# Kernel optimization log

Measured on AMD Instinct MI355X. Metric: run time of the kernel, lower is better.

Reference implementation:

```python
import jax, jax.numpy as jnp
import numpy as np

HEADS = 6
WIN = 7
SHIFT = 3
NEG = -100.0


def _rel_index():
    # Swin relative position index, [49, 49] int
    coords = np.stack(np.meshgrid(np.arange(WIN), np.arange(WIN), indexing='ij')).reshape(2, -1)
    rel = (coords[:, :, None] - coords[:, None, :]).transpose(1, 2, 0)
    rel[:, :, 0] += WIN - 1
    rel[:, :, 1] += WIN - 1
    rel[:, :, 0] *= 2 * WIN - 1
    return rel.sum(-1)


def _shift_mask(H, W):
    # additive shift mask per window, [num_windows, 49, 49]
    img = np.zeros([H, W])
    slices = (slice(0, -WIN), slice(-WIN, -SHIFT), slice(-SHIFT, None))
    cnt = 0
    for h in slices:
        for w in slices:
            img[h, w] = cnt
            cnt += 1
    mw = img.reshape(H // WIN, WIN, W // WIN, WIN).transpose(0, 2, 1, 3).reshape(-1, WIN * WIN)
    diff = mw[:, None, :] - mw[:, :, None]
    return np.where(diff != 0, NEG, 0.0).astype(np.float32)


def setup_inputs() -> dict:
    key = jax.random.key(0)
    ks = jax.random.split(key, 6)
    B, H, W, C = 64, 56, 56, 192
    return {
        'x': jax.random.normal(ks[0], (B, H, W, C), jnp.float32),
        'qkv_w': jax.random.normal(ks[1], (C, 3 * C), jnp.float32) * 0.02,
        'qkv_b': jax.random.normal(ks[2], (3 * C,), jnp.float32) * 0.02,
        'rel_table': jax.random.normal(ks[3], ((2 * WIN - 1) ** 2, HEADS), jnp.float32) * 0.02,
        'proj_w': jax.random.normal(ks[4], (C, C), jnp.float32) * 0.02,
        'proj_b': jax.random.normal(ks[5], (C,), jnp.float32) * 0.02,
    }


def reference(x, qkv_w, qkv_b, rel_table, proj_w, proj_b):
    B, H, W, C = x.shape
    hd = C // HEADS
    scale = hd ** -0.5
    mask = jnp.asarray(_shift_mask(H, W))            # [nW, N, N]
    idx = _rel_index().reshape(-1)                   # static numpy [N*N]

    # cyclic shift + window partition
    xs = jnp.roll(x, (-SHIFT, -SHIFT), (1, 2))
    xw = xs.reshape(B, H // WIN, WIN, W // WIN, WIN, C)
    xw = xw.transpose(0, 1, 3, 2, 4, 5).reshape(-1, WIN * WIN, C)  # [Bn, N, C]
    Bn, N, _ = xw.shape

    qkv = (xw @ qkv_w + qkv_b).reshape(Bn, N, 3, HEADS, hd).transpose(2, 0, 3, 1, 4)
    q, k, v = qkv[0] * scale, qkv[1], qkv[2]         # [Bn, h, N, hd]

    attn = jax.nn.softmax(jnp.einsum('bhnd,bhmd->bhnm', q, k), axis=-1)

    # NOTE: original module adds relative bias and shift mask AFTER softmax
    bias = rel_table[idx].reshape(N, N, HEADS).transpose(2, 0, 1)  # [h, N, N]
    attn = attn + bias[None]
    nW = mask.shape[0]
    attn = (attn.reshape(Bn // nW, nW, HEADS, N, N) + mask[None, :, None]).reshape(Bn, HEADS, N, N)

    out = jnp.einsum('bhnm,bhmd->bhnd', attn, v).transpose(0, 2, 1, 3).reshape(Bn, N, C)
    out = out @ proj_w + proj_b

    # window reverse + un-shift
    out = out.reshape(B, H // WIN, W // WIN, WIN, WIN, C)
    out = out.transpose(0, 1, 3, 2, 4, 5).reshape(B, H, W, C)
    return jnp.roll(out, (SHIFT, SHIFT), (1, 2))
```

## Files before the change

kernel.cpp:

```cpp
#include <hip/hip_runtime.h>
#include <hip/hip_bf16.h>

typedef __attribute__((ext_vector_type(8))) short bf16x8_t;
typedef __attribute__((ext_vector_type(4))) short bf16x4_t;
typedef __attribute__((ext_vector_type(4))) float f32x4_t;

#define MFMA16 __builtin_amdgcn_mfma_f32_16x16x32_bf16

#if __has_builtin(__builtin_amdgcn_mfma_f32_16x16x16bf16_1k)
#define HAVE_MFMA_K16 1
#define MFMA16K16 __builtin_amdgcn_mfma_f32_16x16x16bf16_1k
#else
#define HAVE_MFMA_K16 0
#endif

__device__ __forceinline__ unsigned short f2bf(float f) {
    return __builtin_bit_cast(unsigned short, __float2bfloat16(f));
}
__device__ __forceinline__ int cvt_pk_bf16(float lo, float hi) {
    int r;
    asm("v_cvt_pk_bf16_f32 %0, %1, %2" : "=v"(r) : "v"(lo), "v"(hi));
    return r;
}

__device__ __forceinline__ void group_barrier(int* cnt, int target, int ln) {
    asm volatile("s_waitcnt lgkmcnt(0)" ::: "memory");
    if (ln == 0)
        __hip_atomic_fetch_add(cnt, 1, __ATOMIC_RELEASE, __HIP_MEMORY_SCOPE_WORKGROUP);
    while (__hip_atomic_load(cnt, __ATOMIC_ACQUIRE, __HIP_MEMORY_SCOPE_WORKGROUP) < target)
        __builtin_amdgcn_s_sleep(1);
    __builtin_amdgcn_sched_barrier(0);
}

#define GRP_STRIDE 49152
#define ROWOFF_OFF 98304
#define BAR_OFF    98816
#define SMEM_BYTES 98832

__device__ __forceinline__ int qk_byte(int row, int d) {
    return row * 64 + ((((d >> 3) ^ ((row >> 1) & 3)) << 4) | ((d & 7) << 1));
}
__device__ __forceinline__ int vt_byte(int d, int tok) {
    return d * 128 + ((((tok >> 3) ^ (d & 7)) << 4) | ((tok & 7) << 1));
}

__global__ void prep_weights(const float* __restrict__ qkv_w, const float* __restrict__ proj_w,
                             unsigned short* __restrict__ wqkvT, unsigned short* __restrict__ wprojT)
{
    int i = blockIdx.x * 256 + threadIdx.x;
    if (i < 576 * 192) {
        int n = i / 192, k = i - n * 192;
        wqkvT[i] = f2bf(qkv_w[k * 576 + n]);
    }
    if (i < 192 * 192) {
        int n = i / 192, k = i - n * 192;
        wprojT[i] = f2bf(proj_w[k * 192 + n]);
    }
}

__global__ void prep_bias(const float* __restrict__ rel_table, float* __restrict__ biasT)
{
    int i = blockIdx.x * 256 + threadIdx.x;
    if (i >= 4 * 6 * 16 * 64) return;
    int ln  = i & 63;
    int f   = (i >> 6) & 15;
    int h   = (i >> 10) % 6;
    int wt  = i / 6144;
    int l15 = ln & 15, lg = ln >> 4;
    int mk  = f >> 2, nq = f & 3;
    int qt  = nq * 16 + l15;
    bool bh = (wt & 2) != 0, bw = (wt & 1) != 0;
    float4 o = {0.f, 0.f, 0.f, 0.f};
    float* po = (float*)&o;
    int iq = qt / 7, jq = qt - iq * 7;
    int regq = (bh ? ((iq < 4) ? 3 : 6) : 0) + (bw ? ((jq < 4) ? 1 : 2) : 0);
    for (int r = 0; r < 4; ++r) {
        int kt = mk * 16 + lg * 4 + r;
        if (kt < 49 && qt < 49) {
            int ik = kt / 7, jk = kt - ik * 7;
            int idx = (iq - ik + 6) * 13 + (jq - jk + 6);
            int regk = (bh ? ((ik < 4) ? 3 : 6) : 0) + (bw ? ((jk < 4) ? 1 : 2) : 0);
            po[r] = rel_table[idx * 6 + h] + ((regk != regq) ? -100.0f : 0.0f);
        }
    }
    ((float4*)biasT)[i] = o;
}

__global__ __launch_bounds__(768, 3)
void swin_fused(const float* __restrict__ x,
                const float* __restrict__ qkv_b,
                const float* __restrict__ proj_b,
                const unsigned short* __restrict__ wqkvT,
                const unsigned short* __restrict__ wprojT,
                const float* __restrict__ biasT,
                float* __restrict__ out)
{
    __shared__ unsigned char smem[SMEM_BYTES];

    const int tid = threadIdx.x;
    const int wv  = tid >> 6;
    const int g   = (wv >= 6) ? 1 : 0;
    const int h   = wv - 6 * g;
    const int ln  = tid & 63;
    const int l15 = ln & 15;
    const int lg  = ln >> 4;
    const int tg  = tid - g * 384;

    const int bw  = blockIdx.x * 2 + g;
    const int b   = bw >> 6;
    const int win = bw & 63;
    const int wh  = win >> 3;
    const int ww  = win & 7;
    const int wt  = ((wh == 7) ? 2 : 0) | ((ww == 7) ? 1 : 0);

    const unsigned gbase = g * GRP_STRIDE;
    const unsigned hbase = gbase + h * 8192;
    int* rowOff = (int*)(smem + ROWOFF_OFF + g * 256);
    int* bar    = (int*)(smem + BAR_OFF) + g;
    const f32x4_t zero4 = {0.f, 0.f, 0.f, 0.f};

    if (tid < 2) ((int*)(smem + BAR_OFF))[tid] = 0;
    __syncthreads();

#pragma unroll
    for (int it = 0; it < 8; ++it) {
        int idx = tg + it * 384;
        int n   = idx / 48;
        int c4  = idx - n * 48;
        int2* dst = (int2*)(smem + gbase + n * 400 + c4 * 8);
        if (n < 49) {
            int i = n / 7, j = n - i * 7;
            int sh = wh * 7 + i + 3; if (sh >= 56) sh -= 56;
            int sw = ww * 7 + j + 3; if (sw >= 56) sw -= 56;
            int ro = ((b * 56 + sh) * 56 + sw) * 192;
            if (c4 == 0) rowOff[n] = ro;
            const float4* src = (const float4*)(x + ro + c4 * 4);
            float4 v = *src;
            int2 p;
            p.x = cvt_pk_bf16(v.x, v.y);
            p.y = cvt_pk_bf16(v.z, v.w);
            *dst = p;
        } else {
            *dst = make_int2(0, 0);
        }
    }
    group_barrier(bar, 6, ln);

    f32x4_t accq[4][6];
#pragma unroll
    for (int mt = 0; mt < 4; ++mt)
#pragma unroll
        for (int nt = 0; nt < 6; ++nt) accq[mt][nt] = zero4;
#pragma unroll
    for (int ks = 0; ks < 6; ++ks) {
        bf16x8_t af[4];
#pragma unroll
        for (int mt = 0; mt < 4; ++mt)
            af[mt] = *(const bf16x8_t*)(smem + gbase + (mt * 16 + l15) * 400 + (ks * 32 + lg * 8) * 2);
        bf16x8_t bfv[6];
#pragma unroll
        for (int nt = 0; nt < 6; ++nt)
            bfv[nt] = *(const bf16x8_t*)(wqkvT + ((nt >> 1) * 192 + h * 32 + (nt & 1) * 16 + l15) * 192 + ks * 32 + lg * 8);
        __builtin_amdgcn_s_setprio(1);
#pragma unroll
        for (int nt = 0; nt < 6; ++nt)
#pragma unroll
            for (int mt = 0; mt < 4; ++mt)
                accq[mt][nt] = MFMA16(af[mt], bfv[nt], accq[mt][nt], 0, 0, 0);
        __builtin_amdgcn_s_setprio(0);
    }
    int vbf[4][2][2];
#pragma unroll
    for (int nv = 0; nv < 2; ++nv) {
        float bb = qkv_b[384 + h * 32 + nv * 16 + l15];
#pragma unroll
        for (int mt = 0; mt < 4; ++mt) {
            vbf[mt][nv][0] = cvt_pk_bf16(accq[mt][4 + nv][0] + bb, accq[mt][4 + nv][1] + bb);
            vbf[mt][nv][1] = cvt_pk_bf16(accq[mt][4 + nv][2] + bb, accq[mt][4 + nv][3] + bb);
        }
    }
    group_barrier(bar, 12, ln);

#pragma unroll
    for (int nt = 0; nt < 4; ++nt) {
        int part = nt >> 1;
        int d    = (nt & 1) * 16 + l15;
        float bb = qkv_b[part * 192 + h * 32 + d];
        unsigned base = hbase + part * 4096;
#pragma unroll
        for (int mt = 0; mt < 4; ++mt)
#pragma unroll
            for (int r = 0; r < 4; ++r) {
                int row = mt * 16 + lg * 4 + r;
                *(unsigned short*)(smem + base + qk_byte(row, d)) = f2bf(accq[mt][nt][r] + bb);
            }
    }
    __builtin_amdgcn_sched_barrier(0);

    f32x4_t s[4][4];
    {
        bf16x8_t kf[4], qf[4];
#pragma unroll
        for (int mk = 0; mk < 4; ++mk) {
            int row = mk * 16 + l15;
            kf[mk] = *(const bf16x8_t*)(smem + hbase + 4096 + row * 64 + ((lg ^ ((row >> 1) & 3)) << 4));
        }
#pragma unroll
        for (int nq = 0; nq < 4; ++nq) {
            int row = nq * 16 + l15;
            qf[nq] = *(const bf16x8_t*)(smem + hbase + row * 64 + ((lg ^ ((row >> 1) & 3)) << 4));
        }
        __builtin_amdgcn_s_setprio(1);
#pragma unroll
        for (int mk = 0; mk < 4; ++mk)
#pragma unroll
            for (int nq = 0; nq < 4; ++nq)
                s[mk][nq] = MFMA16(kf[mk], qf[nq], zero4, 0, 0, 0);
        __builtin_amdgcn_s_setprio(0);
    }
    __builtin_amdgcn_sched_barrier(0);

#pragma unroll
    for (int nv = 0; nv < 2; ++nv) {
        int d = nv * 16 + l15;
#pragma unroll
        for (int mt = 0; mt < 4; ++mt) {
            int tok = mt * 16 + lg * 4;
            *(int2*)(smem + hbase + vt_byte(d, tok)) = make_int2(vbf[mt][nv][0], vbf[mt][nv][1]);
        }
    }

    float4 bv4[4][4];
    {
        const float4* bp = (const float4*)biasT + (wt * 6 + h) * 16 * 64 + ln;
#pragma unroll
        for (int mk = 0; mk < 4; ++mk)
#pragma unroll
            for (int nq = 0; nq < 4; ++nq)
                bv4[mk][nq] = bp[(mk * 4 + nq) * 64];
    }

    const float C = 0.17677669529663687f * 1.4426950408889634f;
    int w[4][4][2];
#pragma unroll
    for (int nq = 0; nq < 4; ++nq) {
        float sum = 0.f;
#pragma unroll
        for (int mk = 0; mk < 4; ++mk)
#pragma unroll
            for (int r = 0; r < 4; ++r) {
                int kt = mk * 16 + lg * 4 + r;
                float e = (kt < 49) ? __builtin_amdgcn_exp2f(C * s[mk][nq][r]) : 0.0f;
                s[mk][nq][r] = e;
                sum += e;
            }
        sum += __shfl_xor(sum, 16);
        sum += __shfl_xor(sum, 32);
        float inv = __builtin_amdgcn_rcpf(sum);
#pragma unroll
        for (int mk = 0; mk < 4; ++mk) {
            float v0 = fmaf(s[mk][nq][0], inv, bv4[mk][nq].x);
            float v1 = fmaf(s[mk][nq][1], inv, bv4[mk][nq].y);
            float v2 = fmaf(s[mk][nq][2], inv, bv4[mk][nq].z);
            float v3 = fmaf(s[mk][nq][3], inv, bv4[mk][nq].w);
            w[mk][nq][0] = cvt_pk_bf16(v0, v1);
            w[mk][nq][1] = cvt_pk_bf16(v2, v3);
        }
    }

    f32x4_t o[2][4];
#pragma unroll
    for (int md = 0; md < 2; ++md)
#pragma unroll
        for (int nq = 0; nq < 4; ++nq) o[md][nq] = zero4;

#if HAVE_MFMA_K16
#pragma unroll
    for (int mk = 0; mk < 4; ++mk) {
        bf16x4_t vt2[2];
#pragma unroll
        for (int md = 0; md < 2; ++md) {
            int d = md * 16 + l15;
            vt2[md] = *(const bf16x4_t*)(smem + hbase + vt_byte(d, mk * 16 + lg * 4));
        }
        __builtin_amdgcn_s_setprio(1);
#pragma unroll
        for (int nq = 0; nq < 4; ++nq) {
            bf16x4_t wb = __builtin_bit_cast(bf16x4_t, make_int2(w[mk][nq][0], w[mk][nq][1]));
#pragma unroll
            for (int md = 0; md < 2; ++md)
                o[md][nq] = MFMA16K16(vt2[md], wb, o[md][nq], 0, 0, 0);
        }
        __builtin_amdgcn_s_setprio(0);
    }
#else
    const unsigned Abase = hbase + 4096;
#pragma unroll
    for (int ks = 0; ks < 2; ++ks) {
#pragma unroll
        for (int mh = 0; mh < 2; ++mh) {
            int mk = ks * 2 + mh;
            int d  = mh * 16 + lg * 4;
#pragma unroll
            for (int nq = 0; nq < 4; ++nq) {
                int qt = nq * 16 + l15;
                *(int2*)(smem + Abase + qk_byte(qt, d)) = make_int2(w[mk][nq][0], w[mk][nq][1]);
            }
        }
        __builtin_amdgcn_sched_barrier(0);
        bf16x8_t vf[2], bfr[4];
#pragma unroll
        for (int md = 0; md < 2; ++md) {
            int d = md * 16 + l15;
            vf[md] = *(const bf16x8_t*)(smem + hbase + d * 128 + (((ks * 4 + lg) ^ (d & 7)) << 4));
        }
#pragma unroll
        for (int nq = 0; nq < 4; ++nq) {
            int qt = nq * 16 + l15;
            bfr[nq] = *(const bf16x8_t*)(smem + Abase + qt * 64 + ((lg ^ ((qt >> 1) & 3)) << 4));
        }
        __builtin_amdgcn_s_setprio(1);
#pragma unroll
        for (int nq = 0; nq < 4; ++nq)
#pragma unroll
            for (int md = 0; md < 2; ++md)
                o[md][nq] = MFMA16(vf[md], bfr[nq], o[md][nq], 0, 0, 0);
        __builtin_amdgcn_s_setprio(0);
        __builtin_amdgcn_sched_barrier(0);
    }
#endif
    group_barrier(bar, 18, ln);

#pragma unroll
    for (int md = 0; md < 2; ++md)
#pragma unroll
        for (int nq = 0; nq < 4; ++nq) {
            int qt = nq * 16 + l15;
            int ch = h * 32 + md * 16 + lg * 4;
            int d0 = cvt_pk_bf16(o[md][nq][0], o[md][nq][1]);
            int d1 = cvt_pk_bf16(o[md][nq][2], o[md][nq][3]);
            *(int2*)(smem + gbase + qt * 400 + ch * 2) = make_int2(d0, d1);
        }
    group_barrier(bar, 24, ln);

    f32x4_t y[4][2];
#pragma unroll
    for (int mt = 0; mt < 4; ++mt) { y[mt][0] = zero4; y[mt][1] = zero4; }
#pragma unroll
    for (int ks = 0; ks < 6; ++ks) {
        bf16x8_t aa[4], bb[2];
#pragma unroll
        for (int mt = 0; mt < 4; ++mt)
            aa[mt] = *(const bf16x8_t*)(smem + gbase + (mt * 16 + l15) * 400 + (ks * 32 + lg * 8) * 2);
#pragma unroll
        for (int nt = 0; nt < 2; ++nt)
            bb[nt] = *(const bf16x8_t*)(wprojT + (h * 32 + nt * 16 + l15) * 192 + ks * 32 + lg * 8);
        __builtin_amdgcn_s_setprio(1);
#pragma unroll
        for (int mt = 0; mt < 4; ++mt)
#pragma unroll
            for (int nt = 0; nt < 2; ++nt)
                y[mt][nt] = MFMA16(aa[mt], bb[nt], y[mt][nt], 0, 0, 0);
        __builtin_amdgcn_s_setprio(0);
    }
    float pb0 = proj_b[h * 32 + l15];
    float pb1 = proj_b[h * 32 + 16 + l15];
#pragma unroll
    for (int mt = 0; mt < 4; ++mt)
#pragma unroll
        for (int r = 0; r < 4; ++r) {
            int row = mt * 16 + lg * 4 + r;
            if (row < 49) {
                int ro = rowOff[row];
                out[ro + h * 32 + l15]      = y[mt][0][r] + pb0;
                out[ro + h * 32 + 16 + l15] = y[mt][1][r] + pb1;
            }
        }
}

extern "C" void kernel_launch(void* const* d_in, const int* in_sizes, int n_in,
                              void* d_out, int out_size, void* d_ws, size_t ws_size,
                              hipStream_t stream) {
    const float* x         = (const float*)d_in[0];
    const float* qkv_w     = (const float*)d_in[1];
    const float* qkv_b     = (const float*)d_in[2];
    const float* rel_table = (const float*)d_in[3];
    const float* proj_w    = (const float*)d_in[4];
    const float* proj_b    = (const float*)d_in[5];
    float* out = (float*)d_out;

    unsigned short* wqkvT  = (unsigned short*)d_ws;
    unsigned short* wprojT = wqkvT + 576 * 192;
    float* biasT = (float*)((char*)d_ws + 294912);

    prep_weights<<<576, 256, 0, stream>>>(qkv_w, proj_w, wqkvT, wprojT);
    prep_bias<<<96, 256, 0, stream>>>(rel_table, biasT);
    swin_fused<<<2048, 768, 0, stream>>>(x, qkv_b, proj_b, wqkvT, wprojT, biasT, out);
}
```

Before: 231.5 us.

## Make fused Swin kernel persistent with register prefetch of next window input

The launch shrinks from 2048 to 256 blocks, and each block loops over 8 batch images for the same pair of windows. A separate LDS buffer for the x tile plus a double-buffered row-offset table lets the global loads for the next iteration be issued into registers during the current iteration's output and projection phase. The intent is to hide global load latency and spread launch and setup cost over more work. In exchange, LDS use grows to about 150KB (one block per CU), register pressure rises from the 8 float4 prefetch registers, and only 256 blocks run, which may under-fill the GPU.

```diff
diff --git a/kernel.cpp b/kernel.cpp
--- a/kernel.cpp
+++ b/kernel.cpp
@@ -32,10 +32,11 @@
     __builtin_amdgcn_sched_barrier(0);
 }
 
-#define GRP_STRIDE 49152
-#define ROWOFF_OFF 98304
-#define BAR_OFF    98816
-#define SMEM_BYTES 98832
+#define XB_OFF     98304
+#define ROWOFF_OFF 149504
+#define BAR_OFF    150528
+#define SMEM_BYTES 150536
+#define NIT 8
 
 __device__ __forceinline__ int qk_byte(int row, int d) {
     return row * 64 + ((((d >> 3) ^ ((row >> 1) & 3)) << 4) | ((d & 7) << 1));
@@ -106,276 +107,301 @@
     const int lg  = ln >> 4;
     const int tg  = tid - g * 384;
 
-    const int bw  = blockIdx.x * 2 + g;
-    const int b   = bw >> 6;
-    const int win = bw & 63;
+    const int bx2 = blockIdx.x * 2 + g;
+    const int b0  = bx2 >> 6;
+    const int win = bx2 & 63;
     const int wh  = win >> 3;
     const int ww  = win & 7;
     const int wt  = ((wh == 7) ? 2 : 0) | ((ww == 7) ? 1 : 0);
 
-    const unsigned gbase = g * GRP_STRIDE;
+    const unsigned gbase = g * 49152;
     const unsigned hbase = gbase + h * 8192;
-    int* rowOff = (int*)(smem + ROWOFF_OFF + g * 256);
-    int* bar    = (int*)(smem + BAR_OFF) + g;
+    const unsigned xb    = XB_OFF + g * 25600;
+    int* bar = (int*)(smem + BAR_OFF) + g;
     const f32x4_t zero4 = {0.f, 0.f, 0.f, 0.f};
+    const float4* bp = (const float4*)biasT + (wt * 6 + h) * 16 * 64 + ln;
 
     if (tid < 2) ((int*)(smem + BAR_OFF))[tid] = 0;
     __syncthreads();
 
 #pragma unroll
-    for (int it = 0; it < 8; ++it) {
-        int idx = tg + it * 384;
+    for (int c = 0; c < 8; ++c) {
+        int idx = tg + c * 384;
         int n   = idx / 48;
         int c4  = idx - n * 48;
-        int2* dst = (int2*)(smem + gbase + n * 400 + c4 * 8);
-        if (n < 49) {
-            int i = n / 7, j = n - i * 7;
-            int sh = wh * 7 + i + 3; if (sh >= 56) sh -= 56;
-            int sw = ww * 7 + j + 3; if (sw >= 56) sw -= 56;
-            int ro = ((b * 56 + sh) * 56 + sw) * 192;
-            if (c4 == 0) rowOff[n] = ro;
-            const float4* src = (const float4*)(x + ro + c4 * 4);
-            float4 v = *src;
-            int2 p;
-            p.x = cvt_pk_bf16(v.x, v.y);
-            p.y = cvt_pk_bf16(v.z, v.w);
-            *dst = p;
-        } else {
-            *dst = make_int2(0, 0);
-        }
+        if (n >= 49) *(int2*)(smem + xb + n * 400 + c4 * 8) = make_int2(0, 0);
     }
-    group_barrier(bar, 6, ln);
-
-    f32x4_t accq[4][6];
-#pragma unroll
-    for (int mt = 0; mt < 4; ++mt)
-#pragma unroll
-        for (int nt = 0; nt < 6; ++nt) accq[mt][nt] = zero4;
-#pragma unroll
-    for (int ks = 0; ks < 6; ++ks) {
-        bf16x8_t af[4];
+
+    float4 xr[8];
+    auto prefetch = [&](int itn) {
+        const int bn = itn * 8 + b0;
+        int* rowOffN = (int*)(smem + ROWOFF_OFF + (g * 2 + (itn & 1)) * 256);
+#pragma unroll
+        for (int c = 0; c < 8; ++c) {
+            int idx = tg + c * 384;
+            int n   = idx / 48;
+            int c4  = idx - n * 48;
+            if (n < 49) {
+                int i = n / 7, j = n - i * 7;
+                int sh = wh * 7 + i + 3; if (sh >= 56) sh -= 56;
+                int sw = ww * 7 + j + 3; if (sw >= 56) sw -= 56;
+                int ro = ((bn * 56 + sh) * 56 + sw) * 192;
+                if (c4 == 0) rowOffN[n] = ro;
+                xr[c] = *(const float4*)(x + ro + c4 * 4);
+            }
+        }
+    };
+    prefetch(0);
+
+#pragma unroll 1
+    for (int it = 0; it < NIT; ++it) {
+        const int p  = it & 1;
+        const int tb = it * 18;
+
+#pragma unroll
+        for (int c = 0; c < 8; ++c) {
+            int idx = tg + c * 384;
+            int n   = idx / 48;
+            int c4  = idx - n * 48;
+            if (n < 49) {
+                int2 pk;
+                pk.x = cvt_pk_bf16(xr[c].x, xr[c].y);
+                pk.y = cvt_pk_bf16(xr[c].z, xr[c].w);
+                *(int2*)(smem + xb + n * 400 + c4 * 8) = pk;
+            }
+        }
+        group_barrier(bar, tb + 6, ln);
+
+        f32x4_t accq[4][6];
 #pragma unroll
         for (int mt = 0; mt < 4; ++mt)
-            af[mt] = *(const bf16x8_t*)(smem + gbase + (mt * 16 + l15) * 400 + (ks * 32 + lg * 8) * 2);
-        bf16x8_t bfv[6];
-#pragma unroll
-        for (int nt = 0; nt < 6; ++nt)
-            bfv[nt] = *(const bf16x8_t*)(wqkvT + ((nt >> 1) * 192 + h * 32 + (nt & 1) * 16 + l15) * 192 + ks * 32 + lg * 8);
-        __builtin_amdgcn_s_setprio(1);
-#pragma unroll
-        for (int nt = 0; nt < 6; ++nt)
+#pragma unroll
+            for (int nt = 0; nt < 6; ++nt) accq[mt][nt] = zero4;
+#pragma unroll
+        for (int ks = 0; ks < 6; ++ks) {
+            bf16x8_t af[4];
 #pragma unroll
             for (int mt = 0; mt < 4; ++mt)
-                accq[mt][nt] = MFMA16(af[mt], bfv[nt], accq[mt][nt], 0, 0, 0);
-        __builtin_amdgcn_s_setprio(0);
-    }
-    int vbf[4][2][2];
-#pragma unroll
-    for (int nv = 0; nv < 2; ++nv) {
-        float bb = qkv_b[384 + h * 32 + nv * 16 + l15];
-#pragma unroll
-        for (int mt = 0; mt < 4; ++mt) {
-            vbf[mt][nv][0] = cvt_pk_bf16(accq[mt][4 + nv][0] + bb, accq[mt][4 + nv][1] + bb);
-            vbf[mt][nv][1] = cvt_pk_bf16(accq[mt][4 + nv][2] + bb, accq[mt][4 + nv][3] + bb);
-        }
-    }
-    group_barrier(bar, 12, ln);
-
-#pragma unroll
-    for (int nt = 0; nt < 4; ++nt) {
-        int part = nt >> 1;
-        int d    = (nt & 1) * 16 + l15;
-        float bb = qkv_b[part * 192 + h * 32 + d];
-        unsigned base = hbase + part * 4096;
+                af[mt] = *(const bf16x8_t*)(smem + xb + (mt * 16 + l15) * 400 + (ks * 32 + lg * 8) * 2);
+            bf16x8_t bfv[6];
+#pragma unroll
+            for (int nt = 0; nt < 6; ++nt)
+                bfv[nt] = *(const bf16x8_t*)(wqkvT + ((nt >> 1) * 192 + h * 32 + (nt & 1) * 16 + l15) * 192 + ks * 32 + lg * 8);
+            __builtin_amdgcn_s_setprio(1);
+#pragma unroll
+            for (int nt = 0; nt < 6; ++nt)
+#pragma unroll
+                for (int mt = 0; mt < 4; ++mt)
+                    accq[mt][nt] = MFMA16(af[mt], bfv[nt], accq[mt][nt], 0, 0, 0);
+            __builtin_amdgcn_s_setprio(0);
+        }
+        int vbf[4][2][2];
+#pragma unroll
+        for (int nv = 0; nv < 2; ++nv) {
+            float bb = qkv_b[384 + h * 32 + nv * 16 + l15];
+#pragma unroll
+            for (int mt = 0; mt < 4; ++mt) {
+                vbf[mt][nv][0] = cvt_pk_bf16(accq[mt][4 + nv][0] + bb, accq[mt][4 + nv][1] + bb);
+                vbf[mt][nv][1] = cvt_pk_bf16(accq[mt][4 + nv][2] + bb, accq[mt][4 + nv][3] + bb);
+            }
+        }
+
+#pragma unroll
+        for (int nt = 0; nt < 4; ++nt) {
+            int part = nt >> 1;
+            int d    = (nt & 1) * 16 + l15;
+            float bb = qkv_b[part * 192 + h * 32 + d];
+            unsigned base = hbase + part * 4096;
+#pragma unroll
+            for (int mt = 0; mt < 4; ++mt)
+#pragma unroll
+                for (int r = 0; r < 4; ++r) {
+                    int row = mt * 16 + lg * 4 + r;
+                    *(unsigned short*)(smem + base + qk_byte(row, d)) = f2bf(accq[mt][nt][r] + bb);
+                }
+        }
+        __builtin_amdgcn_sched_barrier(0);
+
+        f32x4_t s[4][4];
+        {
+            bf16x8_t kf[4], qf[4];
+#pragma unroll
+            for (int mk = 0; mk < 4; ++mk) {
+                int row = mk * 16 + l15;
+                kf[mk] = *(const bf16x8_t*)(smem + hbase + 4096 + row * 64 + ((lg ^ ((row >> 1) & 3)) << 4));
+            }
+#pragma unroll
+            for (int nq = 0; nq < 4; ++nq) {
+                int row = nq * 16 + l15;
+                qf[nq] = *(const bf16x8_t*)(smem + hbase + row * 64 + ((lg ^ ((row >> 1) & 3)) << 4));
+            }
+            __builtin_amdgcn_s_setprio(1);
+#pragma unroll
+            for (int mk = 0; mk < 4; ++mk)
+#pragma unroll
+                for (int nq = 0; nq < 4; ++nq)
+                    s[mk][nq] = MFMA16(kf[mk], qf[nq], zero4, 0, 0, 0);
+            __builtin_amdgcn_s_setprio(0);
+        }
+        __builtin_amdgcn_sched_barrier(0);
+
+#pragma unroll
+        for (int nv = 0; nv < 2; ++nv) {
+            int d = nv * 16 + l15;
+#pragma unroll
+            for (int mt = 0; mt < 4; ++mt) {
+                int tok = mt * 16 + lg * 4;
+                *(int2*)(smem + hbase + vt_byte(d, tok)) = make_int2(vbf[mt][nv][0], vbf[mt][nv][1]);
+            }
+        }
+
+        float4 bv4[4][4];
+#pragma unroll
+        for (int mk = 0; mk < 4; ++mk)
+#pragma unroll
+            for (int nq = 0; nq < 4; ++nq)
+                bv4[mk][nq] = bp[(mk * 4 + nq) * 64];
+
+        const float C = 0.17677669529663687f * 1.4426950408889634f;
+        int w[4][4][2];
+#pragma unroll
+        for (int nq = 0; nq < 4; ++nq) {
+            float sum = 0.f;
+#pragma unroll
+            for (int mk = 0; mk < 4; ++mk)
+#pragma unroll
+                for (int r = 0; r < 4; ++r) {
+                    int kt = mk * 16 + lg * 4 + r;
+                    float e = (kt < 49) ? __builtin_amdgcn_exp2f(C * s[mk][nq][r]) : 0.0f;
+                    s[mk][nq][r] = e;
+                    sum += e;
+                }
+            sum += __shfl_xor(sum, 16);
+            sum += __shfl_xor(sum, 32);
+            float inv = __builtin_amdgcn_rcpf(sum);
+#pragma unroll
+            for (int mk = 0; mk < 4; ++mk) {
+                float v0 = fmaf(s[mk][nq][0], inv, bv4[mk][nq].x);
+                float v1 = fmaf(s[mk][nq][1], inv, bv4[mk][nq].y);
+                float v2 = fmaf(s[mk][nq][2], inv, bv4[mk][nq].z);
+                float v3 = fmaf(s[mk][nq][3], inv, bv4[mk][nq].w);
+                w[mk][nq][0] = cvt_pk_bf16(v0, v1);
+                w[mk][nq][1] = cvt_pk_bf16(v2, v3);
+            }
+        }
+
+        f32x4_t o[2][4];
+#pragma unroll
+        for (int md = 0; md < 2; ++md)
+#pragma unroll
+            for (int nq = 0; nq < 4; ++nq) o[md][nq] = zero4;
+
+#if HAVE_MFMA_K16
+#pragma unroll
+        for (int mk = 0; mk < 4; ++mk) {
+            bf16x4_t vt2[2];
+#pragma unroll
+            for (int md = 0; md < 2; ++md) {
+                int d = md * 16 + l15;
+                vt2[md] = *(const bf16x4_t*)(smem + hbase + vt_byte(d, mk * 16 + lg * 4));
+            }
+            __builtin_amdgcn_s_setprio(1);
+#pragma unroll
+            for (int nq = 0; nq < 4; ++nq) {
+                bf16x4_t wb = __builtin_bit_cast(bf16x4_t, make_int2(w[mk][nq][0], w[mk][nq][1]));
+#pragma unroll
+                for (int md = 0; md < 2; ++md)
+                    o[md][nq] = MFMA16K16(vt2[md], wb, o[md][nq], 0, 0, 0);
+            }
+            __builtin_amdgcn_s_setprio(0);
+        }
+#else
+        const unsigned Abase = hbase + 4096;
+#pragma unroll
+        for (int ks = 0; ks < 2; ++ks) {
+#pragma unroll
+            for (int mh = 0; mh < 2; ++mh) {
+                int mk = ks * 2 + mh;
+                int d  = mh * 16 + lg * 4;
+#pragma unroll
+                for (int nq = 0; nq < 4; ++nq) {
+                    int qt = nq * 16 + l15;
+                    *(int2*)(smem + Abase + qk_byte(qt, d)) = make_int2(w[mk][nq][0], w[mk][nq][1]);
+                }
+            }
+            __builtin_amdgcn_sched_barrier(0);
+            bf16x8_t vf[2], bfr[4];
+#pragma unroll
+            for (int md = 0; md < 2; ++md) {
+                int d = md * 16 + l15;
+                vf[md] = *(const bf16x8_t*)(smem + hbase + d * 128 + (((ks * 4 + lg) ^ (d & 7)) << 4));
+            }
+#pragma unroll
+            for (int nq = 0; nq < 4; ++nq) {
+                int qt = nq * 16 + l15;
+                bfr[nq] = *(const bf16x8_t*)(smem + Abase + qt * 64 + ((lg ^ ((qt >> 1) & 3)) << 4));
+            }
+            __builtin_amdgcn_s_setprio(1);
+#pragma unroll
+            for (int nq = 0; nq < 4; ++nq)
+#pragma unroll
+                for (int md = 0; md < 2; ++md)
+                    o[md][nq] = MFMA16(vf[md], bfr[nq], o[md][nq], 0, 0, 0);
+            __builtin_amdgcn_s_setprio(0);
+            __builtin_amdgcn_sched_barrier(0);
+        }
+#endif
+        group_barrier(bar, tb + 12, ln);
+
+        if (it + 1 < NIT) prefetch(it + 1);
+
+#pragma unroll
+        for (int md = 0; md < 2; ++md)
+#pragma unroll
+            for (int nq = 0; nq < 4; ++nq) {
+                int qt = nq * 16 + l15;
+                int ch = h * 32 + md * 16 + lg * 4;
+                int d0 = cvt_pk_bf16(o[md][nq][0], o[md][nq][1]);
+                int d1 = cvt_pk_bf16(o[md][nq][2], o[md][nq][3]);
+                *(int2*)(smem + gbase + qt * 400 + ch * 2) = make_int2(d0, d1);
+            }
+        group_barrier(bar, tb + 18, ln);
+
+        f32x4_t y[4][2];
+#pragma unroll
+        for (int mt = 0; mt < 4; ++mt) { y[mt][0] = zero4; y[mt][1] = zero4; }
+#pragma unroll
+        for (int ks = 0; ks < 6; ++ks) {
+            bf16x8_t aa[4], bb[2];
+#pragma unroll
+            for (int mt = 0; mt < 4; ++mt)
+                aa[mt] = *(const bf16x8_t*)(smem + gbase + (mt * 16 + l15) * 400 + (ks * 32 + lg * 8) * 2);
+#pragma unroll
+            for (int nt = 0; nt < 2; ++nt)
+                bb[nt] = *(const bf16x8_t*)(wprojT + (h * 32 + nt * 16 + l15) * 192 + ks * 32 + lg * 8);
+            __builtin_amdgcn_s_setprio(1);
+#pragma unroll
+            for (int mt = 0; mt < 4; ++mt)
+#pragma unroll
+                for (int nt = 0; nt < 2; ++nt)
+                    y[mt][nt] = MFMA16(aa[mt], bb[nt], y[mt][nt], 0, 0, 0);
+            __builtin_amdgcn_s_setprio(0);
+        }
+        int* rowOff = (int*)(smem + ROWOFF_OFF + (g * 2 + p) * 256);
+        float pb0 = proj_b[h * 32 + l15];
+        float pb1 = proj_b[h * 32 + 16 + l15];
 #pragma unroll
         for (int mt = 0; mt < 4; ++mt)
 #pragma unroll
             for (int r = 0; r < 4; ++r) {
                 int row = mt * 16 + lg * 4 + r;
-                *(unsigned short*)(smem + base + qk_byte(row, d)) = f2bf(accq[mt][nt][r] + bb);
+                if (row < 49) {
+                    int ro = rowOff[row];
+                    out[ro + h * 32 + l15]      = y[mt][0][r] + pb0;
+                    out[ro + h * 32 + 16 + l15] = y[mt][1][r] + pb1;
+                }
             }
     }
-    __builtin_amdgcn_sched_barrier(0);
-
-    f32x4_t s[4][4];
-    {
-        bf16x8_t kf[4], qf[4];
-#pragma unroll
-        for (int mk = 0; mk < 4; ++mk) {
-            int row = mk * 16 + l15;
-            kf[mk] = *(const bf16x8_t*)(smem + hbase + 4096 + row * 64 + ((lg ^ ((row >> 1) & 3)) << 4));
-        }
-#pragma unroll
-        for (int nq = 0; nq < 4; ++nq) {
-            int row = nq * 16 + l15;
-            qf[nq] = *(const bf16x8_t*)(smem + hbase + row * 64 + ((lg ^ ((row >> 1) & 3)) << 4));
-        }
-        __builtin_amdgcn_s_setprio(1);
-#pragma unroll
-        for (int mk = 0; mk < 4; ++mk)
-#pragma unroll
-            for (int nq = 0; nq < 4; ++nq)
-                s[mk][nq] = MFMA16(kf[mk], qf[nq], zero4, 0, 0, 0);
-        __builtin_amdgcn_s_setprio(0);
-    }
-    __builtin_amdgcn_sched_barrier(0);
-
-#pragma unroll
-    for (int nv = 0; nv < 2; ++nv) {
-        int d = nv * 16 + l15;
-#pragma unroll
-        for (int mt = 0; mt < 4; ++mt) {
-            int tok = mt * 16 + lg * 4;
-            *(int2*)(smem + hbase + vt_byte(d, tok)) = make_int2(vbf[mt][nv][0], vbf[mt][nv][1]);
-        }
-    }
-
-    float4 bv4[4][4];
-    {
-        const float4* bp = (const float4*)biasT + (wt * 6 + h) * 16 * 64 + ln;
-#pragma unroll
-        for (int mk = 0; mk < 4; ++mk)
-#pragma unroll
-            for (int nq = 0; nq < 4; ++nq)
-                bv4[mk][nq] = bp[(mk * 4 + nq) * 64];
-    }
-
-    const float C = 0.17677669529663687f * 1.4426950408889634f;
-    int w[4][4][2];
-#pragma unroll
-    for (int nq = 0; nq < 4; ++nq) {
-        float sum = 0.f;
-#pragma unroll
-        for (int mk = 0; mk < 4; ++mk)
-#pragma unroll
-            for (int r = 0; r < 4; ++r) {
-                int kt = mk * 16 + lg * 4 + r;
-                float e = (kt < 49) ? __builtin_amdgcn_exp2f(C * s[mk][nq][r]) : 0.0f;
-                s[mk][nq][r] = e;
-                sum += e;
-            }
-        sum += __shfl_xor(sum, 16);
-        sum += __shfl_xor(sum, 32);
-        float inv = __builtin_amdgcn_rcpf(sum);
-#pragma unroll
-        for (int mk = 0; mk < 4; ++mk) {
-            float v0 = fmaf(s[mk][nq][0], inv, bv4[mk][nq].x);
-            float v1 = fmaf(s[mk][nq][1], inv, bv4[mk][nq].y);
-            float v2 = fmaf(s[mk][nq][2], inv, bv4[mk][nq].z);
-            float v3 = fmaf(s[mk][nq][3], inv, bv4[mk][nq].w);
-            w[mk][nq][0] = cvt_pk_bf16(v0, v1);
-            w[mk][nq][1] = cvt_pk_bf16(v2, v3);
-        }
-    }
-
-    f32x4_t o[2][4];
-#pragma unroll
-    for (int md = 0; md < 2; ++md)
-#pragma unroll
-        for (int nq = 0; nq < 4; ++nq) o[md][nq] = zero4;
-
-#if HAVE_MFMA_K16
-#pragma unroll
-    for (int mk = 0; mk < 4; ++mk) {
-        bf16x4_t vt2[2];
-#pragma unroll
-        for (int md = 0; md < 2; ++md) {
-            int d = md * 16 + l15;
-            vt2[md] = *(const bf16x4_t*)(smem + hbase + vt_byte(d, mk * 16 + lg * 4));
-        }
-        __builtin_amdgcn_s_setprio(1);
-#pragma unroll
-        for (int nq = 0; nq < 4; ++nq) {
-            bf16x4_t wb = __builtin_bit_cast(bf16x4_t, make_int2(w[mk][nq][0], w[mk][nq][1]));
-#pragma unroll
-            for (int md = 0; md < 2; ++md)
-                o[md][nq] = MFMA16K16(vt2[md], wb, o[md][nq], 0, 0, 0);
-        }
-        __builtin_amdgcn_s_setprio(0);
-    }
-#else
-    const unsigned Abase = hbase + 4096;
-#pragma unroll
-    for (int ks = 0; ks < 2; ++ks) {
-#pragma unroll
-        for (int mh = 0; mh < 2; ++mh) {
-            int mk = ks * 2 + mh;
-            int d  = mh * 16 + lg * 4;
-#pragma unroll
-            for (int nq = 0; nq < 4; ++nq) {
-                int qt = nq * 16 + l15;
-                *(int2*)(smem + Abase + qk_byte(qt, d)) = make_int2(w[mk][nq][0], w[mk][nq][1]);
-            }
-        }
-        __builtin_amdgcn_sched_barrier(0);
-        bf16x8_t vf[2], bfr[4];
-#pragma unroll
-        for (int md = 0; md < 2; ++md) {
-            int d = md * 16 + l15;
-            vf[md] = *(const bf16x8_t*)(smem + hbase + d * 128 + (((ks * 4 + lg) ^ (d & 7)) << 4));
-        }
-#pragma unroll
-        for (int nq = 0; nq < 4; ++nq) {
-            int qt = nq * 16 + l15;
-            bfr[nq] = *(const bf16x8_t*)(smem + Abase + qt * 64 + ((lg ^ ((qt >> 1) & 3)) << 4));
-        }
-        __builtin_amdgcn_s_setprio(1);
-#pragma unroll
-        for (int nq = 0; nq < 4; ++nq)
-#pragma unroll
-            for (int md = 0; md < 2; ++md)
-                o[md][nq] = MFMA16(vf[md], bfr[nq], o[md][nq], 0, 0, 0);
-        __builtin_amdgcn_s_setprio(0);
-        __builtin_amdgcn_sched_barrier(0);
-    }
-#endif
-    group_barrier(bar, 18, ln);
-
-#pragma unroll
-    for (int md = 0; md < 2; ++md)
-#pragma unroll
-        for (int nq = 0; nq < 4; ++nq) {
-            int qt = nq * 16 + l15;
-            int ch = h * 32 + md * 16 + lg * 4;
-            int d0 = cvt_pk_bf16(o[md][nq][0], o[md][nq][1]);
-            int d1 = cvt_pk_bf16(o[md][nq][2], o[md][nq][3]);
-            *(int2*)(smem + gbase + qt * 400 + ch * 2) = make_int2(d0, d1);
-        }
-    group_barrier(bar, 24, ln);
-
-    f32x4_t y[4][2];
-#pragma unroll
-    for (int mt = 0; mt < 4; ++mt) { y[mt][0] = zero4; y[mt][1] = zero4; }
-#pragma unroll
-    for (int ks = 0; ks < 6; ++ks) {
-        bf16x8_t aa[4], bb[2];
-#pragma unroll
-        for (int mt = 0; mt < 4; ++mt)
-            aa[mt] = *(const bf16x8_t*)(smem + gbase + (mt * 16 + l15) * 400 + (ks * 32 + lg * 8) * 2);
-#pragma unroll
-        for (int nt = 0; nt < 2; ++nt)
-            bb[nt] = *(const bf16x8_t*)(wprojT + (h * 32 + nt * 16 + l15) * 192 + ks * 32 + lg * 8);
-        __builtin_amdgcn_s_setprio(1);
-#pragma unroll
-        for (int mt = 0; mt < 4; ++mt)
-#pragma unroll
-            for (int nt = 0; nt < 2; ++nt)
-                y[mt][nt] = MFMA16(aa[mt], bb[nt], y[mt][nt], 0, 0, 0);
-        __builtin_amdgcn_s_setprio(0);
-    }
-    float pb0 = proj_b[h * 32 + l15];
-    float pb1 = proj_b[h * 32 + 16 + l15];
-#pragma unroll
-    for (int mt = 0; mt < 4; ++mt)
-#pragma unroll
-        for (int r = 0; r < 4; ++r) {
-            int row = mt * 16 + lg * 4 + r;
-            if (row < 49) {
-                int ro = rowOff[row];
-                out[ro + h * 32 + l15]      = y[mt][0][r] + pb0;
-                out[ro + h * 32 + 16 + l15] = y[mt][1][r] + pb1;
-            }
-        }
 }
 
 extern "C" void kernel_launch(void* const* d_in, const int* in_sizes, int n_in,
@@ -395,5 +421,5 @@
 
     prep_weights<<<576, 256, 0, stream>>>(qkv_w, proj_w, wqkvT, wprojT);
     prep_bias<<<96, 256, 0, stream>>>(rel_table, biasT);
-    swin_fused<<<2048, 768, 0, stream>>>(x, qkv_b, proj_b, wqkvT, wprojT, biasT, out);
-}
+    swin_fused<<<256, 768, 0, stream>>>(x, qkv_b, proj_b, wqkvT, wprojT, biasT, out);
+}
```

Result: slower. 481.2 us (+107.9%).
